# Optimization experiments

Hardware: AMD Instinct MI355X
Metric: run time of the kernel (lower is better)

Reference implementation:

```python
import jax, jax.numpy as jnp
import numpy as np

N = 50000       # num_node
E = 800000      # num edges (avg degree 32)
F_IN, F_HID, F_OUT = 128, 128, 64


def setup_inputs() -> dict:
    key = jax.random.key(0)
    ks = jax.random.split(key, 8)
    x = jax.random.normal(ks[0], (N, F_IN), dtype=jnp.float32)
    edge_index = jax.random.randint(ks[1], (2, E), 0, N, dtype=jnp.int64)
    edge_weight = jax.random.uniform(ks[2], (E,), dtype=jnp.float32)
    s1 = 1.0 / np.sqrt(F_IN)
    s2 = 1.0 / np.sqrt(F_HID)
    W1 = jax.random.normal(ks[3], (F_HID, F_IN), dtype=jnp.float32) * s1
    b1 = jnp.zeros((F_HID,), dtype=jnp.float32)
    W2 = jax.random.normal(ks[4], (F_HID, F_HID), dtype=jnp.float32) * s2
    b2 = jnp.zeros((F_HID,), dtype=jnp.float32)
    W3 = jax.random.normal(ks[5], (F_OUT, F_HID), dtype=jnp.float32) * s2
    b3 = jnp.zeros((F_OUT,), dtype=jnp.float32)
    return {"x": x, "edge_index": edge_index, "edge_weight": edge_weight,
            "W1": W1, "b1": b1, "W2": W2, "b2": b2, "W3": W3, "b3": b3}


def _gcn_norm(edge_index, edge_weight, num_nodes):
    # PyG gcn_norm: add self-loops (weight 1), symmetric D^-1/2 (A+I) D^-1/2
    loop = jnp.arange(num_nodes, dtype=edge_index.dtype)
    row = jnp.concatenate([edge_index[0], loop])  # source
    col = jnp.concatenate([edge_index[1], loop])  # target (aggregation index)
    ew = jnp.concatenate([edge_weight, jnp.ones((num_nodes,), edge_weight.dtype)])
    deg = jax.ops.segment_sum(ew, col, num_segments=num_nodes)
    deg_safe = jnp.where(deg > 0, deg, 1.0)
    dinv = jnp.where(deg > 0, jax.lax.rsqrt(deg_safe), 0.0)
    norm = dinv[row] * ew * dinv[col]  # [E+N]
    return row, col, norm


def reference(x, edge_index, edge_weight, W1, b1, W2, b2, W3, b3):
    num_nodes = x.shape[0]
    row, col, norm = _gcn_norm(edge_index, edge_weight, num_nodes)
    h = x
    for W, b in ((W1, b1), (W2, b2), (W3, b3)):
        m = h @ W.T                                   # [N, d_out]
        msg = m[row] * norm[:, None]                  # gather + scale, [E+N, d_out]
        agg = jax.ops.segment_sum(msg, col, num_segments=num_nodes)
        h = jax.nn.relu(agg + b)                      # GCNConv bias then ReLU
    return h.reshape(-1)                              # torch.flatten
```

## Files before the change

### kernel.cpp

```cpp
#include <hip/hip_runtime.h>
#include <hip/hip_fp16.h>


#define K_DIM 128
#define SCAN_B 256
#define FIXP 1048576.0f
#define HPAD 8

using half8   = __attribute__((ext_vector_type(8))) _Float16;
using floatx4 = __attribute__((ext_vector_type(4))) float;


__global__ void degree_kernel(const int* __restrict__ col, const float* __restrict__ ew,
                              unsigned long long* __restrict__ packed,
                              int* __restrict__ rank, int E) {
    int e = blockIdx.x * blockDim.x + threadIdx.x;
    if (e < E) {
        int c = col[e];
        unsigned long long add = (1ULL << 40) +
            (unsigned long long)(ew[e] * FIXP + 0.5f);
        unsigned long long old = atomicAdd(&packed[(size_t)c * HPAD], add);
        rank[e] = (int)(old >> 40);
    }
}

__global__ void dinv_kernel(const unsigned long long* __restrict__ packed,
                            float* __restrict__ dinv, int* __restrict__ cnt, int n) {
    int i = blockIdx.x * blockDim.x + threadIdx.x;
    if (i < n) {
        unsigned long long p = packed[(size_t)i * HPAD];
        float degw = (float)(p & 0xFFFFFFFFFFULL) * (1.0f / FIXP);
        dinv[i] = rsqrtf(degw + 1.0f);
        cnt[i] = (int)(p >> 40);
    }
}

__global__ void block_reduce_kernel(const int* __restrict__ cnt, int* __restrict__ bsum, int n) {
    __shared__ int s[SCAN_B];
    const int t = threadIdx.x;
    const int i = blockIdx.x * SCAN_B + t;
    s[t] = (i < n) ? cnt[i] + 1 : 0;
    __syncthreads();
    for (int off = SCAN_B / 2; off > 0; off >>= 1) {
        if (t < off) s[t] += s[t + off];
        __syncthreads();
    }
    if (t == 0) bsum[blockIdx.x] = s[0];
}

__global__ void bsum_scan_kernel(int* __restrict__ bsum, int nb) {
    __shared__ int s[SCAN_B];
    const int t = threadIdx.x;
    const int v = (t < nb) ? bsum[t] : 0;
    s[t] = v;
    __syncthreads();
    for (int off = 1; off < SCAN_B; off <<= 1) {
        int u = (t >= off) ? s[t - off] : 0;
        __syncthreads();
        s[t] += u;
        __syncthreads();
    }
    if (t < nb) bsum[t] = s[t] - v;
}

__global__ void scan_write_kernel(const int* __restrict__ cnt,
                                  const int* __restrict__ bsum,
                                  int* __restrict__ offs,
                                  int2* __restrict__ csr, int n) {
    __shared__ int s[SCAN_B];
    const int t = threadIdx.x;
    const int i = blockIdx.x * SCAN_B + t;
    const int v = (i < n) ? cnt[i] + 1 : 0;
    s[t] = v;
    __syncthreads();
    for (int off = 1; off < SCAN_B; off <<= 1) {
        int u = (t >= off) ? s[t - off] : 0;
        __syncthreads();
        s[t] += u;
        __syncthreads();
    }
    const int excl = s[t] - v + bsum[blockIdx.x];
    if (i < n) {
        offs[i] = excl;
        csr[excl] = make_int2(i, __float_as_int(1.0f));
        if (i == n - 1) offs[n] = excl + v;
    }
}

__global__ void fill_kernel(const int* __restrict__ row, const int* __restrict__ col,
                            const float* __restrict__ ew, const int* __restrict__ rank,
                            const int* __restrict__ offs, int2* __restrict__ csr, int E) {
    int e = blockIdx.x * blockDim.x + threadIdx.x;
    if (e < E) {
        int c = col[e];
        int pos = offs[c] + 1 + rank[e];
        csr[pos] = make_int2(row[e], __float_as_int(ew[e]));
    }
}

__global__ void w2h_kernel(const float* __restrict__ W1, const float* __restrict__ W2,
                           const float* __restrict__ W3, __half* __restrict__ Wh,
                           int n1, int n2, int n3) {
    int i = blockIdx.x * blockDim.x + threadIdx.x;
    if (i >= n1 + n2 + n3) return;
    float v = (i < n1) ? W1[i] : (i < n1 + n2 ? W2[i - n1] : W3[i - n1 - n2]);
    Wh[i] = __float2half_rn(v);
}


template <int BN, bool FP32IN>
__global__ __launch_bounds__(256) void mfma_gemm(const void* __restrict__ Ain,
                                                 const __half* __restrict__ Wh,
                                                 const float* __restrict__ dinv,
                                                 __half* __restrict__ C, int nrows) {
    constexpr int NT = BN / 16;
    const int wave = threadIdx.x >> 6;
    const int lane = threadIdx.x & 63;
    const int quad = lane >> 4;
    const int l16  = lane & 15;
    const int row0 = blockIdx.x * 64 + wave * 16;

    int arow = row0 + l16;
    if (arow > nrows - 1) arow = nrows - 1;

    floatx4 acc[NT] = {};

#pragma unroll
    for (int kc = 0; kc < 4; ++kc) {
        const int kof = kc * 32 + quad * 8;
        half8 af;
        if constexpr (FP32IN) {
            const float* ap = (const float*)Ain + (size_t)arow * K_DIM + kof;
            float4 f0 = *(const float4*)ap;
            float4 f1 = *(const float4*)(ap + 4);
            af[0] = (_Float16)f0.x; af[1] = (_Float16)f0.y;
            af[2] = (_Float16)f0.z; af[3] = (_Float16)f0.w;
            af[4] = (_Float16)f1.x; af[5] = (_Float16)f1.y;
            af[6] = (_Float16)f1.z; af[7] = (_Float16)f1.w;
        } else {
            af = *(const half8*)((const __half*)Ain + (size_t)arow * K_DIM + kof);
        }
#pragma unroll
        for (int ct = 0; ct < NT; ++ct) {
            half8 bf = *(const half8*)(Wh + (size_t)(ct * 16 + l16) * K_DIM + kof);
            acc[ct] = __builtin_amdgcn_mfma_f32_16x16x32_f16(af, bf, acc[ct], 0, 0, 0);
        }
    }

    float dv[4];
    int grow[4];
    bool ok[4];
#pragma unroll
    for (int r = 0; r < 4; ++r) {
        grow[r] = row0 + quad * 4 + r;
        ok[r] = grow[r] < nrows;
        dv[r] = ok[r] ? dinv[grow[r]] : 0.f;
    }
#pragma unroll
    for (int ct = 0; ct < NT; ++ct) {
        const int colb = ct * 16 + l16;
#pragma unroll
        for (int r = 0; r < 4; ++r)
            if (ok[r])
                C[(size_t)grow[r] * BN + colb] = __float2half_rn(acc[ct][r] * dv[r]);
    }
}


template <int D, typename OUT>
__global__ __launch_bounds__(256) void agg_kernel(
    const __half* __restrict__ m, const int* __restrict__ offs,
    const int2* __restrict__ csr, const float* __restrict__ dinv,
    const float* __restrict__ bias, OUT* __restrict__ out, int n) {
    const int wid = threadIdx.x >> 6;
    const int lane = threadIdx.x & 63;
    const int node = (blockIdx.x << 2) + wid;
    if (node >= n) return;
    const int beg = offs[node];
    const int end = offs[node + 1];
    const __half2* mh = (const __half2*)m;
    float acc0 = 0.f, acc1 = 0.f;

    if constexpr (D == 128) {
        int k = beg;
        for (; k + 8 <= end; k += 8) {
            int2 e[8];
            float2 f[8];
#pragma unroll
            for (int j = 0; j < 8; ++j) e[j] = csr[k + j];
#pragma unroll
            for (int j = 0; j < 8; ++j)
                f[j] = __half22float2(mh[(size_t)e[j].x * 64 + lane]);
#pragma unroll
            for (int j = 0; j < 8; ++j) {
                float w = __int_as_float(e[j].y);
                acc0 = fmaf(w, f[j].x, acc0);
                acc1 = fmaf(w, f[j].y, acc1);
            }
        }
        for (; k < end; ++k) {
            int2 e0 = csr[k];
            float w0 = __int_as_float(e0.y);
            float2 f0 = __half22float2(mh[(size_t)e0.x * 64 + lane]);
            acc0 = fmaf(w0, f0.x, acc0); acc1 = fmaf(w0, f0.y, acc1);
        }
        const float dv = dinv[node];
        const float2 bv = *(const float2*)(bias + 2 * lane);
        float ox = fmaxf(acc0 * dv + bv.x, 0.f);
        float oy = fmaxf(acc1 * dv + bv.y, 0.f);
        if constexpr (sizeof(OUT) == 2) {
            ((__half2*)out)[(size_t)node * 64 + lane] = __floats2half2_rn(ox, oy);
        } else {
            *(float2*)((float*)out + (size_t)node * 128 + 2 * lane) = make_float2(ox, oy);
        }
    } else {
        const int half = lane >> 5;
        const int sl = lane & 31;
        int k = beg;
        for (; k + 8 <= end; k += 8) {
            int2 e0 = csr[k + half], e1 = csr[k + 2 + half];
            int2 e2 = csr[k + 4 + half], e3 = csr[k + 6 + half];
            float2 f0 = __half22float2(mh[(size_t)e0.x * 32 + sl]);
            float2 f1 = __half22float2(mh[(size_t)e1.x * 32 + sl]);
            float2 f2 = __half22float2(mh[(size_t)e2.x * 32 + sl]);
            float2 f3 = __half22float2(mh[(size_t)e3.x * 32 + sl]);
            float w0 = __int_as_float(e0.y), w1 = __int_as_float(e1.y);
            float w2 = __int_as_float(e2.y), w3 = __int_as_float(e3.y);
            acc0 = fmaf(w0, f0.x, acc0); acc1 = fmaf(w0, f0.y, acc1);
            acc0 = fmaf(w1, f1.x, acc0); acc1 = fmaf(w1, f1.y, acc1);
            acc0 = fmaf(w2, f2.x, acc0); acc1 = fmaf(w2, f2.y, acc1);
            acc0 = fmaf(w3, f3.x, acc0); acc1 = fmaf(w3, f3.y, acc1);
        }
        for (; k + 2 <= end; k += 2) {
            int2 e0 = csr[k + half];
            float w0 = __int_as_float(e0.y);
            float2 f0 = __half22float2(mh[(size_t)e0.x * 32 + sl]);
            acc0 = fmaf(w0, f0.x, acc0); acc1 = fmaf(w0, f0.y, acc1);
        }
        if (k < end && half == 0) {
            int2 e0 = csr[k];
            float w0 = __int_as_float(e0.y);
            float2 f0 = __half22float2(mh[(size_t)e0.x * 32 + sl]);
            acc0 = fmaf(w0, f0.x, acc0); acc1 = fmaf(w0, f0.y, acc1);
        }
        acc0 += __shfl_xor(acc0, 32);
        acc1 += __shfl_xor(acc1, 32);
        if (half == 0) {
            const float dv = dinv[node];
            const float2 bv = *(const float2*)(bias + 2 * sl);
            float ox = fmaxf(acc0 * dv + bv.x, 0.f);
            float oy = fmaxf(acc1 * dv + bv.y, 0.f);
            *(float2*)((float*)out + (size_t)node * 64 + 2 * sl) = make_float2(ox, oy);
        }
    }
}


extern "C" void kernel_launch(void* const* d_in, const int* in_sizes, int n_in,
                              void* d_out, int out_size, void* d_ws, size_t ws_size,
                              hipStream_t stream) {
    const float* x  = (const float*)d_in[0];
    const int*   ei = (const int*)d_in[1];
    const float* ew = (const float*)d_in[2];
    const float* W1 = (const float*)d_in[3];
    const float* b1 = (const float*)d_in[4];
    const float* W2 = (const float*)d_in[5];
    const float* b2 = (const float*)d_in[6];
    const float* W3 = (const float*)d_in[7];
    const float* b3 = (const float*)d_in[8];
    float* out = (float*)d_out;

    const int N = in_sizes[0] / K_DIM;
    const int E = in_sizes[2];
    const int* row = ei;
    const int* col = ei + E;

    const int nb = (N + SCAN_B - 1) / SCAN_B;
    const int NW1 = 128 * 128, NW2 = 128 * 128, NW3 = 64 * 128;

    unsigned long long* packed = (unsigned long long*)d_ws;
    __half* m_buf = (__half*)(packed + (size_t)N * HPAD);
    __half* h_buf = m_buf + (size_t)N * K_DIM;
    __half* Wh    = h_buf + (size_t)N * K_DIM;
    int2*  csr    = (int2*)(Wh + NW1 + NW2 + NW3);
    int*   offs   = (int*)(csr + (size_t)(N + E));
    int*   rank   = offs + (N + 1);
    float* dinv   = (float*)(rank + E);
    int*   cnt    = (int*)(dinv + N);
    int*   bsum   = cnt + N;

    hipMemsetAsync(packed, 0, (size_t)N * HPAD * sizeof(unsigned long long), stream);

    degree_kernel<<<(E + 255) / 256, 256, 0, stream>>>(col, ew, packed, rank, E);
    dinv_kernel<<<(N + 255) / 256, 256, 0, stream>>>(packed, dinv, cnt, N);
    block_reduce_kernel<<<nb, SCAN_B, 0, stream>>>(cnt, bsum, N);
    bsum_scan_kernel<<<1, SCAN_B, 0, stream>>>(bsum, nb);
    scan_write_kernel<<<nb, SCAN_B, 0, stream>>>(cnt, bsum, offs, csr, N);
    fill_kernel<<<(E + 255) / 256, 256, 0, stream>>>(row, col, ew, rank, offs, csr, E);
    w2h_kernel<<<(NW1 + NW2 + NW3 + 255) / 256, 256, 0, stream>>>(W1, W2, W3, Wh,
                                                                  NW1, NW2, NW3);

    const int gemm_blocks = (N + 63) / 64;
    const int agg_blocks = (N + 3) / 4;

    mfma_gemm<128, true><<<gemm_blocks, 256, 0, stream>>>(x, Wh, dinv, m_buf, N);
    agg_kernel<128, __half><<<agg_blocks, 256, 0, stream>>>(m_buf, offs, csr, dinv, b1, h_buf, N);
    mfma_gemm<128, false><<<gemm_blocks, 256, 0, stream>>>(h_buf, Wh + NW1, dinv, m_buf, N);
    agg_kernel<128, __half><<<agg_blocks, 256, 0, stream>>>(m_buf, offs, csr, dinv, b2, h_buf, N);
    mfma_gemm<64, false><<<gemm_blocks, 256, 0, stream>>>(h_buf, Wh + NW1 + NW2, dinv, m_buf, N);
    agg_kernel<64, float><<<agg_blocks, 256, 0, stream>>>(m_buf, offs, csr, dinv, b3, out, N);
}
```

Before: 327.8 us.

## Build CSR via two-pass LDS radix sort of packed edge keys

Replaces the atomic-degree, rank, and scan-based CSR construction with a packed 64-bit edge list (col, row, weight) that is sorted by column in two 8-bit radix passes. Segment boundaries and degrees are then derived from the sorted list. The aim is to remove the contended global 64-bit atomics and the scattered fill writes, at the cost of more kernels and extra passes over an 8-byte-per-edge buffer. Packing row into 16 bits and reading col from bits 48 and up assumes node ids below 65536, which holds for N=50000. Since the sort order within a column is not fixed, the order of floating-point summation may change.

```diff
diff --git a/kernel.cpp b/kernel.cpp
--- a/kernel.cpp
+++ b/kernel.cpp
@@ -3,99 +3,128 @@
 
 
 #define K_DIM 128
-#define SCAN_B 256
-#define FIXP 1048576.0f
-#define HPAD 8
+#define SORT_ITEMS 2048
+
+typedef unsigned long long u64;
+typedef unsigned int u32;
 
 using half8   = __attribute__((ext_vector_type(8))) _Float16;
 using floatx4 = __attribute__((ext_vector_type(4))) float;
 
 
-__global__ void degree_kernel(const int* __restrict__ col, const float* __restrict__ ew,
-                              unsigned long long* __restrict__ packed,
-                              int* __restrict__ rank, int E) {
-    int e = blockIdx.x * blockDim.x + threadIdx.x;
-    if (e < E) {
-        int c = col[e];
-        unsigned long long add = (1ULL << 40) +
-            (unsigned long long)(ew[e] * FIXP + 0.5f);
-        unsigned long long old = atomicAdd(&packed[(size_t)c * HPAD], add);
-        rank[e] = (int)(old >> 40);
-    }
-}
-
-__global__ void dinv_kernel(const unsigned long long* __restrict__ packed,
-                            float* __restrict__ dinv, int* __restrict__ cnt, int n) {
+__global__ void build_kernel(const int* __restrict__ row, const int* __restrict__ col,
+                             const float* __restrict__ ew, u64* __restrict__ el,
+                             int E, int N) {
     int i = blockIdx.x * blockDim.x + threadIdx.x;
-    if (i < n) {
-        unsigned long long p = packed[(size_t)i * HPAD];
-        float degw = (float)(p & 0xFFFFFFFFFFULL) * (1.0f / FIXP);
-        dinv[i] = rsqrtf(degw + 1.0f);
-        cnt[i] = (int)(p >> 40);
-    }
-}
-
-__global__ void block_reduce_kernel(const int* __restrict__ cnt, int* __restrict__ bsum, int n) {
-    __shared__ int s[SCAN_B];
+    if (i < E) {
+        el[i] = ((u64)(u32)col[i] << 48) | ((u64)(u32)row[i] << 32)
+              | (u64)__float_as_uint(ew[i]);
+    } else if (i < E + N) {
+        int v = i - E;
+        el[i] = ((u64)(u32)v << 48) | ((u64)(u32)v << 32)
+              | (u64)__float_as_uint(1.0f);
+    }
+}
+
+__global__ void p1_hist(const u64* __restrict__ el, u32* __restrict__ ghist,
+                        int total, int nb) {
+    __shared__ u32 bin[256];
+    bin[threadIdx.x] = 0;
+    __syncthreads();
+    const int base = blockIdx.x * SORT_ITEMS;
+    const int end = min(base + SORT_ITEMS, total);
+    for (int i = base + threadIdx.x; i < end; i += 256)
+        atomicAdd(&bin[(u32)(el[i] >> 56)], 1u);
+    __syncthreads();
+    ghist[(size_t)threadIdx.x * nb + blockIdx.x] = bin[threadIdx.x];
+}
+
+__global__ void p1_scan(u32* __restrict__ g, u32* __restrict__ dbase, int nb) {
+    __shared__ u32 s[1024];
+    const int tot = 256 * nb;
+    const int C = (tot + 1023) >> 10;
     const int t = threadIdx.x;
-    const int i = blockIdx.x * SCAN_B + t;
-    s[t] = (i < n) ? cnt[i] + 1 : 0;
-    __syncthreads();
-    for (int off = SCAN_B / 2; off > 0; off >>= 1) {
-        if (t < off) s[t] += s[t + off];
+    const int lo = t * C, hi = min(lo + C, tot);
+    u32 sum = 0;
+    for (int i = lo; i < hi; ++i) sum += g[i];
+    s[t] = sum;
+    __syncthreads();
+    for (int off = 1; off < 1024; off <<= 1) {
+        u32 v = (t >= off) ? s[t - off] : 0;
         __syncthreads();
-    }
-    if (t == 0) bsum[blockIdx.x] = s[0];
-}
-
-__global__ void bsum_scan_kernel(int* __restrict__ bsum, int nb) {
-    __shared__ int s[SCAN_B];
+        s[t] += v;
+        __syncthreads();
+    }
+    u32 run = (t == 0) ? 0 : s[t - 1];
+    for (int i = lo; i < hi; ++i) {
+        u32 old = g[i];
+        g[i] = run;
+        if (i % nb == 0) dbase[i / nb] = run;
+        run += old;
+    }
+}
+
+__global__ void p1_scatter(const u64* __restrict__ el, const u32* __restrict__ ghist,
+                           u64* __restrict__ out, int total, int nb) {
+    __shared__ u32 cur[256];
+    cur[threadIdx.x] = ghist[(size_t)threadIdx.x * nb + blockIdx.x];
+    __syncthreads();
+    const int base = blockIdx.x * SORT_ITEMS;
+    const int end = min(base + SORT_ITEMS, total);
+    for (int i = base + threadIdx.x; i < end; i += 256) {
+        u64 e = el[i];
+        u32 p = atomicAdd(&cur[(u32)(e >> 56)], 1u);
+        out[p] = e;
+    }
+}
+
+__global__ void p2_sort(const u64* __restrict__ in, u64* __restrict__ out,
+                        const u32* __restrict__ dbase) {
     const int t = threadIdx.x;
-    const int v = (t < nb) ? bsum[t] : 0;
+    const int base = (int)dbase[blockIdx.x];
+    const int size = (int)dbase[blockIdx.x + 1] - base;
+    __shared__ u32 hist[256], cur[256], s[256];
+    hist[t] = 0;
+    __syncthreads();
+    for (int i = t; i < size; i += 256)
+        atomicAdd(&hist[(u32)(in[base + i] >> 48) & 0xFFu], 1u);
+    __syncthreads();
+    const u32 v = hist[t];
     s[t] = v;
     __syncthreads();
-    for (int off = 1; off < SCAN_B; off <<= 1) {
-        int u = (t >= off) ? s[t - off] : 0;
+    for (int off = 1; off < 256; off <<= 1) {
+        u32 u = (t >= off) ? s[t - off] : 0;
         __syncthreads();
         s[t] += u;
         __syncthreads();
     }
-    if (t < nb) bsum[t] = s[t] - v;
-}
-
-__global__ void scan_write_kernel(const int* __restrict__ cnt,
-                                  const int* __restrict__ bsum,
-                                  int* __restrict__ offs,
-                                  int2* __restrict__ csr, int n) {
-    __shared__ int s[SCAN_B];
-    const int t = threadIdx.x;
-    const int i = blockIdx.x * SCAN_B + t;
-    const int v = (i < n) ? cnt[i] + 1 : 0;
-    s[t] = v;
-    __syncthreads();
-    for (int off = 1; off < SCAN_B; off <<= 1) {
-        int u = (t >= off) ? s[t - off] : 0;
-        __syncthreads();
-        s[t] += u;
-        __syncthreads();
-    }
-    const int excl = s[t] - v + bsum[blockIdx.x];
-    if (i < n) {
-        offs[i] = excl;
-        csr[excl] = make_int2(i, __float_as_int(1.0f));
-        if (i == n - 1) offs[n] = excl + v;
-    }
-}
-
-__global__ void fill_kernel(const int* __restrict__ row, const int* __restrict__ col,
-                            const float* __restrict__ ew, const int* __restrict__ rank,
-                            const int* __restrict__ offs, int2* __restrict__ csr, int E) {
-    int e = blockIdx.x * blockDim.x + threadIdx.x;
-    if (e < E) {
-        int c = col[e];
-        int pos = offs[c] + 1 + rank[e];
-        csr[pos] = make_int2(row[e], __float_as_int(ew[e]));
-    }
+    cur[t] = (u32)base + s[t] - v;
+    __syncthreads();
+    for (int i = t; i < size; i += 256) {
+        u64 e = in[base + i];
+        u32 p = atomicAdd(&cur[(u32)(e >> 48) & 0xFFu], 1u);
+        out[p] = e;
+    }
+}
+
+__global__ void boundary_kernel(const u64* __restrict__ el, int* __restrict__ offs,
+                                int total, int n) {
+    int i = blockIdx.x * blockDim.x + threadIdx.x;
+    if (i >= total) return;
+    int c = (int)(el[i] >> 48);
+    if (i == 0 || c != (int)(el[i - 1] >> 48)) offs[c] = i;
+    if (i == 0) offs[n] = total;
+}
+
+__global__ void dinv_kernel(const u64* __restrict__ el, const int* __restrict__ offs,
+                            float* __restrict__ dinv, int n) {
+    int i = blockIdx.x * blockDim.x + threadIdx.x;
+    if (i >= n) return;
+    const int b = offs[i], e = offs[i + 1];
+    float s = 0.f;
+    for (int k = b; k < e; ++k)
+        s += __uint_as_float((u32)(el[k] & 0xFFFFFFFFu));
+    dinv[i] = rsqrtf(s);
 }
 
 __global__ void w2h_kernel(const float* __restrict__ W1, const float* __restrict__ W2,
@@ -190,18 +219,18 @@
             for (int j = 0; j < 8; ++j) e[j] = csr[k + j];
 #pragma unroll
             for (int j = 0; j < 8; ++j)
-                f[j] = __half22float2(mh[(size_t)e[j].x * 64 + lane]);
+                f[j] = __half22float2(mh[(size_t)(e[j].y & 0xFFFF) * 64 + lane]);
 #pragma unroll
             for (int j = 0; j < 8; ++j) {
-                float w = __int_as_float(e[j].y);
+                float w = __int_as_float(e[j].x);
                 acc0 = fmaf(w, f[j].x, acc0);
                 acc1 = fmaf(w, f[j].y, acc1);
             }
         }
         for (; k < end; ++k) {
             int2 e0 = csr[k];
-            float w0 = __int_as_float(e0.y);
-            float2 f0 = __half22float2(mh[(size_t)e0.x * 64 + lane]);
+            float w0 = __int_as_float(e0.x);
+            float2 f0 = __half22float2(mh[(size_t)(e0.y & 0xFFFF) * 64 + lane]);
             acc0 = fmaf(w0, f0.x, acc0); acc1 = fmaf(w0, f0.y, acc1);
         }
         const float dv = dinv[node];
@@ -220,12 +249,12 @@
         for (; k + 8 <= end; k += 8) {
             int2 e0 = csr[k + half], e1 = csr[k + 2 + half];
             int2 e2 = csr[k + 4 + half], e3 = csr[k + 6 + half];
-            float2 f0 = __half22float2(mh[(size_t)e0.x * 32 + sl]);
-            float2 f1 = __half22float2(mh[(size_t)e1.x * 32 + sl]);
-            float2 f2 = __half22float2(mh[(size_t)e2.x * 32 + sl]);
-            float2 f3 = __half22float2(mh[(size_t)e3.x * 32 + sl]);
-            float w0 = __int_as_float(e0.y), w1 = __int_as_float(e1.y);
-            float w2 = __int_as_float(e2.y), w3 = __int_as_float(e3.y);
+            float2 f0 = __half22float2(mh[(size_t)(e0.y & 0xFFFF) * 32 + sl]);
+            float2 f1 = __half22float2(mh[(size_t)(e1.y & 0xFFFF) * 32 + sl]);
+            float2 f2 = __half22float2(mh[(size_t)(e2.y & 0xFFFF) * 32 + sl]);
+            float2 f3 = __half22float2(mh[(size_t)(e3.y & 0xFFFF) * 32 + sl]);
+            float w0 = __int_as_float(e0.x), w1 = __int_as_float(e1.x);
+            float w2 = __int_as_float(e2.x), w3 = __int_as_float(e3.x);
             acc0 = fmaf(w0, f0.x, acc0); acc1 = fmaf(w0, f0.y, acc1);
             acc0 = fmaf(w1, f1.x, acc0); acc1 = fmaf(w1, f1.y, acc1);
             acc0 = fmaf(w2, f2.x, acc0); acc1 = fmaf(w2, f2.y, acc1);
@@ -233,14 +262,14 @@
         }
         for (; k + 2 <= end; k += 2) {
             int2 e0 = csr[k + half];
-            float w0 = __int_as_float(e0.y);
-            float2 f0 = __half22float2(mh[(size_t)e0.x * 32 + sl]);
+            float w0 = __int_as_float(e0.x);
+            float2 f0 = __half22float2(mh[(size_t)(e0.y & 0xFFFF) * 32 + sl]);
             acc0 = fmaf(w0, f0.x, acc0); acc1 = fmaf(w0, f0.y, acc1);
         }
         if (k < end && half == 0) {
             int2 e0 = csr[k];
-            float w0 = __int_as_float(e0.y);
-            float2 f0 = __half22float2(mh[(size_t)e0.x * 32 + sl]);
+            float w0 = __int_as_float(e0.x);
+            float2 f0 = __half22float2(mh[(size_t)(e0.y & 0xFFFF) * 32 + sl]);
             acc0 = fmaf(w0, f0.x, acc0); acc1 = fmaf(w0, f0.y, acc1);
         }
         acc0 += __shfl_xor(acc0, 32);
@@ -275,33 +304,34 @@
     const int* row = ei;
     const int* col = ei + E;
 
-    const int nb = (N + SCAN_B - 1) / SCAN_B;
+    const int total = E + N;
+    const int nb = (total + SORT_ITEMS - 1) / SORT_ITEMS;
+    const int ngroups = (N + 255) >> 8;
     const int NW1 = 128 * 128, NW2 = 128 * 128, NW3 = 64 * 128;
 
-    unsigned long long* packed = (unsigned long long*)d_ws;
-    __half* m_buf = (__half*)(packed + (size_t)N * HPAD);
+    u64* elA      = (u64*)d_ws;
+    u64* elB      = elA + total;
+    __half* m_buf = (__half*)(elB + total);
     __half* h_buf = m_buf + (size_t)N * K_DIM;
     __half* Wh    = h_buf + (size_t)N * K_DIM;
-    int2*  csr    = (int2*)(Wh + NW1 + NW2 + NW3);
-    int*   offs   = (int*)(csr + (size_t)(N + E));
-    int*   rank   = offs + (N + 1);
-    float* dinv   = (float*)(rank + E);
-    int*   cnt    = (int*)(dinv + N);
-    int*   bsum   = cnt + N;
-
-    hipMemsetAsync(packed, 0, (size_t)N * HPAD * sizeof(unsigned long long), stream);
-
-    degree_kernel<<<(E + 255) / 256, 256, 0, stream>>>(col, ew, packed, rank, E);
-    dinv_kernel<<<(N + 255) / 256, 256, 0, stream>>>(packed, dinv, cnt, N);
-    block_reduce_kernel<<<nb, SCAN_B, 0, stream>>>(cnt, bsum, N);
-    bsum_scan_kernel<<<1, SCAN_B, 0, stream>>>(bsum, nb);
-    scan_write_kernel<<<nb, SCAN_B, 0, stream>>>(cnt, bsum, offs, csr, N);
-    fill_kernel<<<(E + 255) / 256, 256, 0, stream>>>(row, col, ew, rank, offs, csr, E);
+    u32* ghist    = (u32*)(Wh + NW1 + NW2 + NW3);
+    u32* dbase    = ghist + (size_t)256 * nb;
+    int* offs     = (int*)(dbase + 257);
+    float* dinv   = (float*)(offs + N + 1);
+
+    build_kernel<<<(total + 255) / 256, 256, 0, stream>>>(row, col, ew, elA, E, N);
+    p1_hist<<<nb, 256, 0, stream>>>(elA, ghist, total, nb);
+    p1_scan<<<1, 1024, 0, stream>>>(ghist, dbase, nb);
+    p1_scatter<<<nb, 256, 0, stream>>>(elA, ghist, elB, total, nb);
+    p2_sort<<<ngroups, 256, 0, stream>>>(elB, elA, dbase);
+    boundary_kernel<<<(total + 255) / 256, 256, 0, stream>>>(elA, offs, total, N);
+    dinv_kernel<<<(N + 255) / 256, 256, 0, stream>>>(elA, offs, dinv, N);
     w2h_kernel<<<(NW1 + NW2 + NW3 + 255) / 256, 256, 0, stream>>>(W1, W2, W3, Wh,
                                                                   NW1, NW2, NW3);
 
     const int gemm_blocks = (N + 63) / 64;
     const int agg_blocks = (N + 3) / 4;
+    const int2* csr = (const int2*)elA;
 
     mfma_gemm<128, true><<<gemm_blocks, 256, 0, stream>>>(x, Wh, dinv, m_buf, N);
     agg_kernel<128, __half><<<agg_blocks, 256, 0, stream>>>(m_buf, offs, csr, dinv, b1, h_buf, N);
```

New measurement: 471.1 us. 43.7% more time.
